# Kernel tuning notes

Hardware: AMD Instinct MI355X
Metric: run time of the kernel (lower is better)

Reference implementation:

```python
import jax, jax.numpy as jnp
import numpy as np

INF = 1e10
D_KEY = 64

def setup_inputs() -> dict:
    key = jax.random.key(0)
    k1, k2, k3 = jax.random.split(key, 3)
    B, S, D = 4, 4096, D_KEY
    return {
        "query": jax.random.normal(k1, (B, S, D), dtype=jnp.float32),
        "key": jax.random.normal(k2, (B, S, D), dtype=jnp.float32),
        "value": jax.random.normal(k3, (B, S, D), dtype=jnp.float32),
        "mask": jnp.ones((B, S), dtype=jnp.float32),
    }

def reference(query, key, value, mask):
    # dot_products: [B, Sq, Sk]
    dot = jnp.einsum('bqd,bkd->bqk', query, key)
    S = key.shape[1]
    # causal: subtract INF on strict upper triangle (triu(1))
    tri = jnp.triu(jnp.ones((S, S), dtype=dot.dtype), 1) * INF
    dot = dot - tri[None, :, :]
    # additive padding mask: subtract (1-mask)*INF broadcast over query dim
    dot = dot - (1.0 - mask)[:, None, :] * INF
    scale = jnp.sqrt(jnp.float32(D_KEY))
    probs = jax.nn.softmax(dot / scale, axis=-1)  # [B, Sq, Sk]
    # dropout ratio = 0.0 -> identity
    return jnp.einsum('bqk,bkd->bqd', probs, value)
```

## Files before the change

kernel.cpp:

```cpp
#include <hip/hip_runtime.h>
#include <hip/hip_bf16.h>


#define S_LEN  4096
#define N_B    4
#define NT64   64
#define BIGF   1.803368e9f
#define QSCALE (0.125f * 1.44269504089f)
#define FIXMAX 11.0f
#define BIGNEG 1.25e9f
#define MADD_PAD 4224

typedef __attribute__((ext_vector_type(8))) short short8;
typedef __attribute__((ext_vector_type(4))) float f32x4;
typedef __attribute__((ext_vector_type(2))) unsigned int uint2v;
typedef unsigned short ushort_t;

#define KT2_OFF   0
#define KT2_BYTES (N_B * NT64 * 4096 * 2)
#define VT2_OFF   (KT2_OFF + KT2_BYTES)
#define VT2_BYTES (N_B * NT64 * 4096 * 2)
#define NSLOT     (N_B * 368 * 4)
#define OP_OFF    (VT2_OFF + VT2_BYTES)
#define OP_BYTES  (NSLOT * 512 * 4)
#define PLS_OFF   (OP_OFF + OP_BYTES)
#define PLS_BYTES (NSLOT * 16 * 4)
#define MADD_OFF  (PLS_OFF + PLS_BYTES)
#define MADD_BYTES (N_B * MADD_PAD * 4)
#define FLAG_OFF  (MADD_OFF + MADD_BYTES)
#define WS5_NEEDED (FLAG_OFF + 64)

__device__ __forceinline__ unsigned short f2bf(float f) {
    union { float f; unsigned u; } v; v.f = f;
    unsigned r = v.u + 0x7FFF + ((v.u >> 16) & 1);
    return (unsigned short)(r >> 16);
}
__device__ __forceinline__ float bflo(unsigned u) {
    union { unsigned u; float f; } v; v.u = u << 16; return v.f;
}
__device__ __forceinline__ float bfhi(unsigned u) {
    union { unsigned u; float f; } v; v.u = u & 0xffff0000u; return v.f;
}
__device__ __forceinline__ void ld_lds16(const void* g, void* l) {
    __builtin_amdgcn_global_load_lds((const __attribute__((address_space(1))) void*)g,
                                     (__attribute__((address_space(3))) void*)l, 16, 0, 0);
}


__global__ __launch_bounds__(256)
void prep5(const float* __restrict__ K, const float* __restrict__ V,
           const float* __restrict__ M,
           ushort_t* __restrict__ Kt, ushort_t* __restrict__ Vt,
           float* __restrict__ Madd, unsigned* __restrict__ Flag)
{
    const int t = blockIdx.x, b = blockIdx.y, tid = threadIdx.x;
    ushort_t* ko = Kt + ((size_t)(b * NT64 + t)) * 4096;
    ushort_t* vo = Vt + ((size_t)(b * NT64 + t)) * 4096;
    #pragma unroll
    for (int i = 0; i < 2; ++i) {
        const int idx = tid + 256 * i;
        const int row = idx >> 3, cc = idx & 7;
        const float* src = K + ((size_t)(b * S_LEN + t * 64 + row)) * 64 + cc * 8;
        const f32x4 a = *(const f32x4*)src;
        const f32x4 d4 = *(const f32x4*)(src + 4);
        short8 w;
        w[0]=(short)f2bf(a[0]); w[1]=(short)f2bf(a[1]); w[2]=(short)f2bf(a[2]); w[3]=(short)f2bf(a[3]);
        w[4]=(short)f2bf(d4[0]); w[5]=(short)f2bf(d4[1]); w[6]=(short)f2bf(d4[2]); w[7]=(short)f2bf(d4[3]);
        *(short8*)(ko + row * 64 + ((cc ^ (row & 7)) << 3)) = w;
    }
    #pragma unroll
    for (int i = 0; i < 2; ++i) {
        const int idx = tid + 256 * i;
        const int cc = idx >> 6, d = idx & 63;
        short8 w;
        #pragma unroll
        for (int j = 0; j < 8; ++j)
            w[j] = (short)f2bf(V[((size_t)(b * S_LEN + t * 64 + cc * 8 + j)) * 64 + d]);
        *(short8*)(vo + d * 64 + ((cc ^ (d & 7)) << 3)) = w;
    }
    if (tid < 64) {
        const int k = t * 64 + tid;
        const float mv = M[b * S_LEN + k];
        Madd[b * MADD_PAD + k] = (1.0f - mv) * BIGF;
        const unsigned long long nz = __ballot(mv != 1.0f);
        if (tid == 0 && nz) atomicOr(Flag, 1u);
    }
}

#define PTRANS(PA, PB, PF) do {                                                     \
    unsigned c00_, c01_, c10_, c11_;                                                \
    __asm__("v_cvt_pk_bf16_f32 %0, %1, %2" : "=v"(c00_) : "v"(PA[0]), "v"(PA[1])); \
    __asm__("v_cvt_pk_bf16_f32 %0, %1, %2" : "=v"(c01_) : "v"(PA[2]), "v"(PA[3])); \
    __asm__("v_cvt_pk_bf16_f32 %0, %1, %2" : "=v"(c10_) : "v"(PB[0]), "v"(PB[1])); \
    __asm__("v_cvt_pk_bf16_f32 %0, %1, %2" : "=v"(c11_) : "v"(PB[2]), "v"(PB[3])); \
    uint2v s0_ = __builtin_amdgcn_permlane32_swap(c00_, c10_, false, false);        \
    uint2v s1_ = __builtin_amdgcn_permlane32_swap(c01_, c11_, false, false);        \
    const unsigned T0_ = (unsigned)__builtin_amdgcn_ds_swizzle((int)s0_.x, 0x401F); \
    const unsigned T1_ = (unsigned)__builtin_amdgcn_ds_swizzle((int)s1_.x, 0x401F); \
    const unsigned U0_ = (unsigned)__builtin_amdgcn_ds_swizzle((int)s0_.y, 0x401F); \
    const unsigned U1_ = (unsigned)__builtin_amdgcn_ds_swizzle((int)s1_.y, 0x401F); \
    union { unsigned u[4]; short8 s; } pw_;                                         \
    pw_.u[0] = evn ? s0_.x : U0_;                                                   \
    pw_.u[1] = evn ? s1_.x : U1_;                                                   \
    pw_.u[2] = evn ? T0_ : s0_.y;                                                   \
    pw_.u[3] = evn ? T1_ : s1_.y;                                                   \
    PF = pw_.s;                                                                     \
} while (0)

__global__ __launch_bounds__(256)
void attn_fa8(const float* __restrict__ Q, const ushort_t* __restrict__ Kt,
              const ushort_t* __restrict__ Vt, const float* __restrict__ Madd,
              const unsigned* __restrict__ Flag,
              unsigned* __restrict__ Opu, float* __restrict__ Pll,
              float* __restrict__ O)
{
    const int x = 373 - blockIdx.x;
    const int b = blockIdx.y;
    int v = 1;
    #pragma unroll
    for (int vv = 2; vv <= 11; ++vv) v += (x >= 3 * vv * (vv - 1)) ? 1 : 0;
    const int y  = x - 3 * v * (v - 1);
    const int T  = 6 * (v - 1) + y / v;
    const int c  = y - (y / v) * v;
    const int t0 = 6 * c;
    const int tmax = T + 1;
    const int t1 = (t0 + 6 < tmax) ? t0 + 6 : tmax;

    const unsigned anymask = *Flag;

    const int wid  = threadIdx.x >> 6;
    const int lane = threadIdx.x & 63, l15 = lane & 15, g = lane >> 4;
    const bool evn = ((lane & 16) == 0);
    const int qbase = T * 64 + wid * 16;

    __shared__ __attribute__((aligned(16))) ushort_t Kb[2][4096];
    __shared__ __attribute__((aligned(16))) ushort_t Vb[2][4096];

    const float* Qrow = Q + ((size_t)(b * S_LEN + qbase + l15)) * 64 + g * 8;
    const f32x4 qa = *(const f32x4*)(Qrow);
    const f32x4 qb_ = *(const f32x4*)(Qrow + 4);
    const f32x4 qc = *(const f32x4*)(Qrow + 32);
    const f32x4 qd = *(const f32x4*)(Qrow + 36);
    short8 qf0, qf1;
    #pragma unroll
    for (int j = 0; j < 4; ++j) {
        qf0[j]     = (short)f2bf(qa[j]  * QSCALE);
        qf0[4 + j] = (short)f2bf(qb_[j] * QSCALE);
        qf1[j]     = (short)f2bf(qc[j]  * QSCALE);
        qf1[4 + j] = (short)f2bf(qd[j]  * QSCALE);
    }
    short8 ones8;
    #pragma unroll
    for (int j = 0; j < 8; ++j) ones8[j] = (short)0x3F80;

    const char*  KtB = (const char*)Kt + (size_t)b * (NT64 * 8192);
    const char*  VtB = (const char*)Vt + (size_t)b * (NT64 * 8192);
    const float* MaB = Madd + (size_t)b * MADD_PAD + 4 * g;

    f32x4 acc[5];
    #pragma unroll
    for (int dt = 0; dt < 5; ++dt) acc[dt] = (f32x4){0.f, 0.f, 0.f, 0.f};

    auto stage = [&](int bf, int t_) {
        const char* kg = KtB + (size_t)t_ * 8192 + wid * 2048 + lane * 16;
        char* kl = (char*)&Kb[bf][0] + wid * 2048;
        ld_lds16(kg,        kl);
        ld_lds16(kg + 1024, kl + 1024);
        const char* vg = VtB + (size_t)t_ * 8192 + wid * 2048 + lane * 16;
        char* vl = (char*)&Vb[bf][0] + wid * 2048;
        ld_lds16(vg,        vl);
        ld_lds16(vg + 1024, vl + 1024);
    };

    stage(0, t0);
    int buf = 0;
    const int ch0 = ((g ^ (l15 & 7)) << 3);
    const int ch1 = (((4 | g) ^ (l15 & 7)) << 3);

    for (int t = t0; t < t1; ++t) {
        f32x4 mm0, mm1, mm2, mm3;
        if (anymask) {
            const float* mp = MaB + t * 64;
            mm0 = *(const f32x4*)(mp);
            mm1 = *(const f32x4*)(mp + 16);
            mm2 = *(const f32x4*)(mp + 32);
            mm3 = *(const f32x4*)(mp + 48);
        }
        if (t + 1 < t1) {
            stage(buf ^ 1, t + 1);
            __asm__ volatile("s_waitcnt vmcnt(4)" ::: "memory");
        } else {
            __asm__ volatile("s_waitcnt vmcnt(0)" ::: "memory");
        }
        __builtin_amdgcn_s_barrier();
        __builtin_amdgcn_sched_barrier(0);

        const ushort_t* kb = &Kb[buf][0];
        const f32x4 z_ = (f32x4){0.f, 0.f, 0.f, 0.f};
        short8 k00 = *(const short8*)(kb + ((0  + l15) << 6) + ch0);
        short8 k01 = *(const short8*)(kb + ((0  + l15) << 6) + ch1);
        short8 k10 = *(const short8*)(kb + ((16 + l15) << 6) + ch0);
        short8 k11 = *(const short8*)(kb + ((16 + l15) << 6) + ch1);
        short8 k20 = *(const short8*)(kb + ((32 + l15) << 6) + ch0);
        short8 k21 = *(const short8*)(kb + ((32 + l15) << 6) + ch1);
        short8 k30 = *(const short8*)(kb + ((48 + l15) << 6) + ch0);
        short8 k31 = *(const short8*)(kb + ((48 + l15) << 6) + ch1);
        f32x4 st0 = __builtin_amdgcn_mfma_f32_16x16x32_bf16(k00, qf0, z_, 0, 0, 0);
        f32x4 st1 = __builtin_amdgcn_mfma_f32_16x16x32_bf16(k10, qf0, z_, 0, 0, 0);
        f32x4 st2 = __builtin_amdgcn_mfma_f32_16x16x32_bf16(k20, qf0, z_, 0, 0, 0);
        f32x4 st3 = __builtin_amdgcn_mfma_f32_16x16x32_bf16(k30, qf0, z_, 0, 0, 0);
        st0 = __builtin_amdgcn_mfma_f32_16x16x32_bf16(k01, qf1, st0, 0, 0, 0);
        st1 = __builtin_amdgcn_mfma_f32_16x16x32_bf16(k11, qf1, st1, 0, 0, 0);
        st2 = __builtin_amdgcn_mfma_f32_16x16x32_bf16(k21, qf1, st2, 0, 0, 0);
        st3 = __builtin_amdgcn_mfma_f32_16x16x32_bf16(k31, qf1, st3, 0, 0, 0);

        if (anymask) {
            st0 -= mm0; st1 -= mm1; st2 -= mm2; st3 -= mm3;
        }
        if (t == T) {
            const int qg = 16 * wid + l15 - 4 * g;
            #pragma unroll
            for (int r = 0; r < 4; ++r) {
                if (r > qg)      st0[r] -= BIGF;
                if (16 + r > qg) st1[r] -= BIGF;
                if (32 + r > qg) st2[r] -= BIGF;
                if (48 + r > qg) st3[r] -= BIGF;
            }
        }

        float p0[4], p1[4], p2[4], p3[4];
        #pragma unroll
        for (int r = 0; r < 4; ++r) {
            p0[r] = exp2f(st0[r] - FIXMAX);
            p1[r] = exp2f(st1[r] - FIXMAX);
            p2[r] = exp2f(st2[r] - FIXMAX);
            p3[r] = exp2f(st3[r] - FIXMAX);
        }

        short8 pfA, pfB;
        PTRANS(p0, p1, pfA);
        PTRANS(p2, p3, pfB);

        const ushort_t* vb = &Vb[buf][0];
        short8 vA0 = *(const short8*)(vb + ((0  + l15) << 6) + ch0);
        short8 vB0 = *(const short8*)(vb + ((0  + l15) << 6) + ch1);
        short8 vA1 = *(const short8*)(vb + ((16 + l15) << 6) + ch0);
        short8 vB1 = *(const short8*)(vb + ((16 + l15) << 6) + ch1);
        short8 vA2 = *(const short8*)(vb + ((32 + l15) << 6) + ch0);
        short8 vB2 = *(const short8*)(vb + ((32 + l15) << 6) + ch1);
        short8 vA3 = *(const short8*)(vb + ((48 + l15) << 6) + ch0);
        short8 vB3 = *(const short8*)(vb + ((48 + l15) << 6) + ch1);
        __builtin_amdgcn_s_setprio(1);
        acc[0] = __builtin_amdgcn_mfma_f32_16x16x32_bf16(pfA, vA0, acc[0], 0, 0, 0);
        acc[1] = __builtin_amdgcn_mfma_f32_16x16x32_bf16(pfA, vA1, acc[1], 0, 0, 0);
        acc[2] = __builtin_amdgcn_mfma_f32_16x16x32_bf16(pfA, vA2, acc[2], 0, 0, 0);
        acc[3] = __builtin_amdgcn_mfma_f32_16x16x32_bf16(pfA, vA3, acc[3], 0, 0, 0);
        acc[4] = __builtin_amdgcn_mfma_f32_16x16x32_bf16(pfA, ones8, acc[4], 0, 0, 0);
        acc[0] = __builtin_amdgcn_mfma_f32_16x16x32_bf16(pfB, vB0, acc[0], 0, 0, 0);
        acc[1] = __builtin_amdgcn_mfma_f32_16x16x32_bf16(pfB, vB1, acc[1], 0, 0, 0);
        acc[2] = __builtin_amdgcn_mfma_f32_16x16x32_bf16(pfB, vB2, acc[2], 0, 0, 0);
        acc[3] = __builtin_amdgcn_mfma_f32_16x16x32_bf16(pfB, vB3, acc[3], 0, 0, 0);
        acc[4] = __builtin_amdgcn_mfma_f32_16x16x32_bf16(pfB, ones8, acc[4], 0, 0, 0);
        __builtin_amdgcn_s_setprio(0);

        __builtin_amdgcn_sched_barrier(0);
        __builtin_amdgcn_s_barrier();
        buf ^= 1;
    }

    if (v == 1) {
        float* Ob = O + ((size_t)(b * S_LEN + qbase)) * 64;
        #pragma unroll
        for (int r = 0; r < 4; ++r) {
            const float il = 1.0f / acc[4][r];
            #pragma unroll
            for (int dt = 0; dt < 4; ++dt)
                Ob[(4 * g + r) * 64 + 16 * dt + l15] = acc[dt][r] * il;
        }
    } else {
        const int slot = (b * 368 + (x - 6)) * 4 + wid;
        unsigned* Os = Opu + (size_t)slot * 512;
        #pragma unroll
        for (int dt = 0; dt < 4; ++dt) {
            unsigned plo, phi;
            __asm__("v_cvt_pk_bf16_f32 %0, %1, %2" : "=v"(plo) : "v"(acc[dt][0]), "v"(acc[dt][1]));
            __asm__("v_cvt_pk_bf16_f32 %0, %1, %2" : "=v"(phi) : "v"(acc[dt][2]), "v"(acc[dt][3]));
            *(uint2v*)&Os[(16 * dt + l15) * 8 + g * 2] = (uint2v){plo, phi};
        }
        if (l15 == 0) {
            #pragma unroll
            for (int r = 0; r < 4; ++r)
                Pll[slot * 16 + 4 * g + r] = acc[4][r];
        }
    }
}

__global__ __launch_bounds__(256)
void combine5(const unsigned* __restrict__ Opu, const float* __restrict__ Pll,
              float* __restrict__ O)
{
    const int bx = blockIdx.x, b = blockIdx.y;
    const int T = 6 + (bx >> 2), w = bx & 3;
    const int v = (T + 6) / 6;
    const int x0 = 3 * v * (v - 1) + (T - 6 * (v - 1)) * v;
    const int sb = (b * 368 + (x0 - 6)) * 4 + w;
    const int tid = threadIdx.x, rg = tid >> 6, d = tid & 63;

    float l[4] = {0.f, 0.f, 0.f, 0.f};
    float a[4] = {0.f, 0.f, 0.f, 0.f};
    for (int cc = 0; cc < v; ++cc) {
        const int sl = sb + 4 * cc;
        #pragma unroll
        for (int j = 0; j < 4; ++j)
            l[j] += Pll[sl * 16 + 4 * rg + j];
        const uint2v pu = *(const uint2v*)&Opu[(size_t)sl * 512 + d * 8 + rg * 2];
        a[0] += bflo(pu[0]);
        a[1] += bfhi(pu[0]);
        a[2] += bflo(pu[1]);
        a[3] += bfhi(pu[1]);
    }
    float* Ob = O + ((size_t)(b * S_LEN + T * 64 + w * 16 + 4 * rg)) * 64 + d;
    #pragma unroll
    for (int j = 0; j < 4; ++j)
        Ob[(size_t)j * 64] = a[j] / l[j];
}


__global__ __launch_bounds__(256)
void attn_fwd_fb(const float* __restrict__ Q, const float* __restrict__ K,
                 const float* __restrict__ V, const float* __restrict__ M,
                 float* __restrict__ O)
{
    const int tile  = blockIdx.x;
    const int b     = blockIdx.y;
    const int qbase = tile * 64;
    const int tid   = threadIdx.x;
    const int wave  = tid >> 6;
    const int lane  = tid & 63;
    const int l15   = lane & 15;
    const int g     = lane >> 4;

    __shared__ __attribute__((aligned(16))) unsigned short Klds[32 * 64];
    __shared__ __attribute__((aligned(16))) unsigned short Vtlds[64 * 40];
    __shared__ __attribute__((aligned(16))) unsigned short Plds[4][16 * 40];

    const float* Qb = Q + ((size_t)b * S_LEN + qbase) * 64;
    const float* Kb = K + (size_t)b * S_LEN * 64;
    const float* Vb = V + (size_t)b * S_LEN * 64;
    const float* Mb = M + (size_t)b * S_LEN;

    const int qrow = 16 * wave + l15;
    short8 qf[2];
    #pragma unroll
    for (int dc = 0; dc < 2; ++dc) {
        const float* src = Qb + (size_t)qrow * 64 + dc * 32 + g * 8;
        #pragma unroll
        for (int j = 0; j < 8; ++j) qf[dc][j] = (short)f2bf(src[j] * 0.125f);
    }

    f32x4 acc[4];
    #pragma unroll
    for (int dt = 0; dt < 4; ++dt) acc[dt] = (f32x4){0.f, 0.f, 0.f, 0.f};
    float mrow[4], lrow[4];
    #pragma unroll
    for (int r = 0; r < 4; ++r) { mrow[r] = -1e30f; lrow[r] = 0.f; }

    const int q_max_wave = qbase + 16 * wave + 15;
    const int nkv = (qbase + 64) / 32;

    for (int it = 0; it < nkv; ++it) {
        const int kv = it * 32;
        __syncthreads();
        {
            const int k = tid >> 3, c = tid & 7;
            const float* src = Kb + (size_t)(kv + k) * 64 + c * 8;
            short8 t8;
            #pragma unroll
            for (int j = 0; j < 8; ++j) t8[j] = (short)f2bf(src[j]);
            const int byte = k * 128 + ((c * 16) ^ ((k & 7) << 4));
            *(short8*)((char*)Klds + byte) = t8;
        }
        {
            const int k = tid & 31, dch = tid >> 5;
            const float* src = Vb + (size_t)(kv + k) * 64 + dch * 8;
            #pragma unroll
            for (int j = 0; j < 8; ++j)
                Vtlds[(dch * 8 + j) * 40 + k] = f2bf(src[j]);
        }
        __syncthreads();

        if (kv > q_max_wave) continue;

        f32x4 s[2];
        s[0] = (f32x4){0.f,0.f,0.f,0.f};
        s[1] = (f32x4){0.f,0.f,0.f,0.f};
        #pragma unroll
        for (int kt = 0; kt < 2; ++kt) {
            const int krow = 16 * kt + l15;
            #pragma unroll
            for (int dc = 0; dc < 2; ++dc) {
                const int byte = krow * 128 + ((dc * 64 + g * 16) ^ ((krow & 7) << 4));
                short8 kf = *(const short8*)((const char*)Klds + byte);
                s[kt] = __builtin_amdgcn_mfma_f32_16x16x32_bf16(qf[dc], kf, s[kt], 0, 0, 0);
            }
        }

        float mk0 = Mb[kv + l15];
        float mk1 = Mb[kv + 16 + l15];
        #pragma unroll
        for (int kt = 0; kt < 2; ++kt) {
            const int gk = kv + 16 * kt + l15;
            const float madd = (1.0f - (kt ? mk1 : mk0)) * BIGNEG;
            #pragma unroll
            for (int r = 0; r < 4; ++r) {
                const int gq = qbase + 16 * wave + 4 * g + r;
                float vv = s[kt][r] - madd;
                if (gk > gq) vv -= BIGNEG;
                s[kt][r] = vv;
            }
        }

        float pexp[2][4], alpha[4];
        #pragma unroll
        for (int r = 0; r < 4; ++r) {
            float tm = fmaxf(s[0][r], s[1][r]);
            #pragma unroll
            for (int off = 8; off >= 1; off >>= 1)
                tm = fmaxf(tm, __shfl_xor(tm, off, 64));
            const float mnew = fmaxf(mrow[r], tm);
            const float a  = __expf(mrow[r] - mnew);
            const float p0 = __expf(s[0][r] - mnew);
            const float p1 = __expf(s[1][r] - mnew);
            float rs = p0 + p1;
            #pragma unroll
            for (int off = 8; off >= 1; off >>= 1)
                rs += __shfl_xor(rs, off, 64);
            lrow[r] = lrow[r] * a + rs;
            mrow[r] = mnew;
            alpha[r] = a;
            pexp[0][r] = p0; pexp[1][r] = p1;
        }

        #pragma unroll
        for (int dt = 0; dt < 4; ++dt)
            #pragma unroll
            for (int r = 0; r < 4; ++r)
                acc[dt][r] *= alpha[r];

        unsigned short* P = Plds[wave];
        #pragma unroll
        for (int kt = 0; kt < 2; ++kt)
            #pragma unroll
            for (int r = 0; r < 4; ++r)
                P[(4 * g + r) * 40 + 16 * kt + l15] = f2bf(pexp[kt][r]);

        __asm__ volatile("s_waitcnt lgkmcnt(0)" ::: "memory");

        short8 pf = *(const short8*)((const char*)P + (l15 * 40 + g * 8) * 2);
        #pragma unroll
        for (int dt = 0; dt < 4; ++dt) {
            short8 vf = *(const short8*)((const char*)Vtlds + ((dt * 16 + l15) * 40 + g * 8) * 2);
            acc[dt] = __builtin_amdgcn_mfma_f32_16x16x32_bf16(pf, vf, acc[dt], 0, 0, 0);
        }
    }

    float* Ob = O + ((size_t)b * S_LEN + qbase) * 64;
    #pragma unroll
    for (int r = 0; r < 4; ++r) {
        const float inv = 1.0f / lrow[r];
        const int row = 16 * wave + 4 * g + r;
        #pragma unroll
        for (int dt = 0; dt < 4; ++dt)
            Ob[(size_t)row * 64 + dt * 16 + l15] = acc[dt][r] * inv;
    }
}

extern "C" void kernel_launch(void* const* d_in, const int* in_sizes, int n_in,
                              void* d_out, int out_size, void* d_ws, size_t ws_size,
                              hipStream_t stream) {
    const float* Q = (const float*)d_in[0];
    const float* K = (const float*)d_in[1];
    const float* V = (const float*)d_in[2];
    const float* M = (const float*)d_in[3];
    float* O = (float*)d_out;

    if (ws_size >= (size_t)WS5_NEEDED) {
        ushort_t* Kt = (ushort_t*)((char*)d_ws + KT2_OFF);
        ushort_t* Vt = (ushort_t*)((char*)d_ws + VT2_OFF);
        unsigned* Op = (unsigned*)((char*)d_ws + OP_OFF);
        float*    Pll= (float*)((char*)d_ws + PLS_OFF);
        float*    Ma = (float*)((char*)d_ws + MADD_OFF);
        unsigned* Fl = (unsigned*)((char*)d_ws + FLAG_OFF);
        hipMemsetAsync(Fl, 0, 4, stream);
        prep5<<<dim3(NT64, N_B), 256, 0, stream>>>(K, V, M, Kt, Vt, Ma, Fl);
        attn_fa8<<<dim3(374, N_B), 256, 0, stream>>>(Q, Kt, Vt, Ma, Fl, Op, Pll, O);
        combine5<<<dim3(232, N_B), 256, 0, stream>>>(Op, Pll, O);
    } else {
        dim3 grid(S_LEN / 64, N_B);
        attn_fwd_fb<<<grid, 256, 0, stream>>>(Q, K, V, M, O);
    }
}
```

Measured before the change: 45.59 us.

## Use 128-row query tiles with 8 waves and a triple-buffered K/V pipeline

Moves the main attention kernel to 512-thread blocks that each cover 128 query rows, so every staged K/V tile is reused by eight waves instead of four, which halves the number of work items. Global-to-LDS staging becomes a three-slot ring with a prefetch distance of two and one barrier per tile. The padding-mask additive is now staged into LDS and always applied, which removes the host memset and the any-mask flag path. Waves whose diagonal tile comes before the block's last tile skip compute on the final tile. The costs are larger blocks with more LDS per block, idle waves on the diagonal, and a changed split and combine layout.

```diff
diff --git a/kernel.cpp b/kernel.cpp
--- a/kernel.cpp
+++ b/kernel.cpp
@@ -20,15 +20,14 @@
 #define KT2_BYTES (N_B * NT64 * 4096 * 2)
 #define VT2_OFF   (KT2_OFF + KT2_BYTES)
 #define VT2_BYTES (N_B * NT64 * 4096 * 2)
-#define NSLOT     (N_B * 368 * 4)
+#define NSLOT     (N_B * 184 * 8)
 #define OP_OFF    (VT2_OFF + VT2_BYTES)
 #define OP_BYTES  (NSLOT * 512 * 4)
 #define PLS_OFF   (OP_OFF + OP_BYTES)
 #define PLS_BYTES (NSLOT * 16 * 4)
 #define MADD_OFF  (PLS_OFF + PLS_BYTES)
 #define MADD_BYTES (N_B * MADD_PAD * 4)
-#define FLAG_OFF  (MADD_OFF + MADD_BYTES)
-#define WS5_NEEDED (FLAG_OFF + 64)
+#define WS8_NEEDED (MADD_OFF + MADD_BYTES)
 
 __device__ __forceinline__ unsigned short f2bf(float f) {
     union { float f; unsigned u; } v; v.f = f;
@@ -45,13 +44,17 @@
     __builtin_amdgcn_global_load_lds((const __attribute__((address_space(1))) void*)g,
                                      (__attribute__((address_space(3))) void*)l, 16, 0, 0);
 }
+__device__ __forceinline__ void ld_lds4(const void* g, void* l) {
+    __builtin_amdgcn_global_load_lds((const __attribute__((address_space(1))) void*)g,
+                                     (__attribute__((address_space(3))) void*)l, 4, 0, 0);
+}
 
 
 __global__ __launch_bounds__(256)
-void prep5(const float* __restrict__ K, const float* __restrict__ V,
+void prep6(const float* __restrict__ K, const float* __restrict__ V,
            const float* __restrict__ M,
            ushort_t* __restrict__ Kt, ushort_t* __restrict__ Vt,
-           float* __restrict__ Madd, unsigned* __restrict__ Flag)
+           float* __restrict__ Madd)
 {
     const int t = blockIdx.x, b = blockIdx.y, tid = threadIdx.x;
     ushort_t* ko = Kt + ((size_t)(b * NT64 + t)) * 4096;
@@ -80,10 +83,7 @@
     }
     if (tid < 64) {
         const int k = t * 64 + tid;
-        const float mv = M[b * S_LEN + k];
-        Madd[b * MADD_PAD + k] = (1.0f - mv) * BIGF;
-        const unsigned long long nz = __ballot(mv != 1.0f);
-        if (tid == 0 && nz) atomicOr(Flag, 1u);
+        Madd[b * MADD_PAD + k] = (1.0f - M[b * S_LEN + k]) * BIGF;
     }
 }
 
@@ -107,40 +107,46 @@
     PF = pw_.s;                                                                     \
 } while (0)
 
-__global__ __launch_bounds__(256)
-void attn_fa8(const float* __restrict__ Q, const ushort_t* __restrict__ Kt,
-              const ushort_t* __restrict__ Vt, const float* __restrict__ Madd,
-              const unsigned* __restrict__ Flag,
-              unsigned* __restrict__ Opu, float* __restrict__ Pll,
-              float* __restrict__ O)
+#define CMASK(SV, BB, QG) do {                     \
+    _Pragma("unroll")                              \
+    for (int r_ = 0; r_ < 4; ++r_)                 \
+        if ((BB) + r_ > (QG)) SV[r_] -= BIGF;      \
+} while (0)
+
+__global__ __launch_bounds__(512, 6)
+void attn_fa11(const float* __restrict__ Q, const ushort_t* __restrict__ Kt,
+               const ushort_t* __restrict__ Vt, const float* __restrict__ Madd,
+               unsigned* __restrict__ Opu, float* __restrict__ Pll,
+               float* __restrict__ O)
 {
-    const int x = 373 - blockIdx.x;
+    const int x = 186 - blockIdx.x;
     const int b = blockIdx.y;
     int v = 1;
     #pragma unroll
-    for (int vv = 2; vv <= 11; ++vv) v += (x >= 3 * vv * (vv - 1)) ? 1 : 0;
-    const int y  = x - 3 * v * (v - 1);
-    const int T  = 6 * (v - 1) + y / v;
+    for (int vv = 2; vv <= 11; ++vv) v += (x >= (3 * vv * (vv - 1)) / 2) ? 1 : 0;
+    const int y  = x - (3 * v * (v - 1)) / 2;
+    const int T  = 3 * (v - 1) + y / v;
     const int c  = y - (y / v) * v;
+    const int nt = 2 * T + 2;
     const int t0 = 6 * c;
-    const int tmax = T + 1;
-    const int t1 = (t0 + 6 < tmax) ? t0 + 6 : tmax;
-
-    const unsigned anymask = *Flag;
+    const int t1 = (t0 + 6 < nt) ? t0 + 6 : nt;
 
     const int wid  = threadIdx.x >> 6;
     const int lane = threadIdx.x & 63, l15 = lane & 15, g = lane >> 4;
     const bool evn = ((lane & 16) == 0);
-    const int qbase = T * 64 + wid * 16;
-
-    __shared__ __attribute__((aligned(16))) ushort_t Kb[2][4096];
-    __shared__ __attribute__((aligned(16))) ushort_t Vb[2][4096];
+    const int qbase = T * 128 + wid * 16;
+    const int dtile = 2 * T + (wid >> 2);
+    const int qg = 16 * (wid & 3) + l15 - 4 * g;
+
+    __shared__ __attribute__((aligned(16))) ushort_t Kb[3][4096];
+    __shared__ __attribute__((aligned(16))) ushort_t Vb[3][4096];
+    __shared__ __attribute__((aligned(16))) float    Ml[3][64];
 
     const float* Qrow = Q + ((size_t)(b * S_LEN + qbase + l15)) * 64 + g * 8;
-    const f32x4 qa = *(const f32x4*)(Qrow);
+    const f32x4 qa  = *(const f32x4*)(Qrow);
     const f32x4 qb_ = *(const f32x4*)(Qrow + 4);
-    const f32x4 qc = *(const f32x4*)(Qrow + 32);
-    const f32x4 qd = *(const f32x4*)(Qrow + 36);
+    const f32x4 qc  = *(const f32x4*)(Qrow + 32);
+    const f32x4 qd  = *(const f32x4*)(Qrow + 36);
     short8 qf0, qf1;
     #pragma unroll
     for (int j = 0; j < 4; ++j) {
@@ -153,119 +159,110 @@
     #pragma unroll
     for (int j = 0; j < 8; ++j) ones8[j] = (short)0x3F80;
 
-    const char*  KtB = (const char*)Kt + (size_t)b * (NT64 * 8192);
-    const char*  VtB = (const char*)Vt + (size_t)b * (NT64 * 8192);
-    const float* MaB = Madd + (size_t)b * MADD_PAD + 4 * g;
+    const char*  KtB  = (const char*)Kt + (size_t)b * (NT64 * 8192);
+    const char*  VtB  = (const char*)Vt + (size_t)b * (NT64 * 8192);
+    const float* MaBs = Madd + (size_t)b * MADD_PAD;
 
     f32x4 acc[5];
     #pragma unroll
     for (int dt = 0; dt < 5; ++dt) acc[dt] = (f32x4){0.f, 0.f, 0.f, 0.f};
 
-    auto stage = [&](int bf, int t_) {
-        const char* kg = KtB + (size_t)t_ * 8192 + wid * 2048 + lane * 16;
-        char* kl = (char*)&Kb[bf][0] + wid * 2048;
-        ld_lds16(kg,        kl);
-        ld_lds16(kg + 1024, kl + 1024);
-        const char* vg = VtB + (size_t)t_ * 8192 + wid * 2048 + lane * 16;
-        char* vl = (char*)&Vb[bf][0] + wid * 2048;
-        ld_lds16(vg,        vl);
-        ld_lds16(vg + 1024, vl + 1024);
+    auto stage = [&](int sl, int t_) {
+        ld_lds16(KtB + (size_t)t_ * 8192 + wid * 1024 + lane * 16,
+                 (char*)&Kb[sl][0] + wid * 1024);
+        ld_lds16(VtB + (size_t)t_ * 8192 + wid * 1024 + lane * 16,
+                 (char*)&Vb[sl][0] + wid * 1024);
+        if (wid == 0)
+            ld_lds4(MaBs + (size_t)t_ * 64 + lane, &Ml[sl][0]);
     };
 
     stage(0, t0);
-    int buf = 0;
+    if (t0 + 1 < t1) stage(1, t0 + 1);
+
     const int ch0 = ((g ^ (l15 & 7)) << 3);
     const int ch1 = (((4 | g) ^ (l15 & 7)) << 3);
 
+    int sc = 0;
     for (int t = t0; t < t1; ++t) {
-        f32x4 mm0, mm1, mm2, mm3;
-        if (anymask) {
-            const float* mp = MaB + t * 64;
-            mm0 = *(const f32x4*)(mp);
-            mm1 = *(const f32x4*)(mp + 16);
-            mm2 = *(const f32x4*)(mp + 32);
-            mm3 = *(const f32x4*)(mp + 48);
-        }
         if (t + 1 < t1) {
-            stage(buf ^ 1, t + 1);
-            __asm__ volatile("s_waitcnt vmcnt(4)" ::: "memory");
+            if (wid == 0) __asm__ volatile("s_waitcnt vmcnt(3)" ::: "memory");
+            else          __asm__ volatile("s_waitcnt vmcnt(2)" ::: "memory");
         } else {
             __asm__ volatile("s_waitcnt vmcnt(0)" ::: "memory");
         }
         __builtin_amdgcn_s_barrier();
         __builtin_amdgcn_sched_barrier(0);
 
-        const ushort_t* kb = &Kb[buf][0];
-        const f32x4 z_ = (f32x4){0.f, 0.f, 0.f, 0.f};
-        short8 k00 = *(const short8*)(kb + ((0  + l15) << 6) + ch0);
-        short8 k01 = *(const short8*)(kb + ((0  + l15) << 6) + ch1);
-        short8 k10 = *(const short8*)(kb + ((16 + l15) << 6) + ch0);
-        short8 k11 = *(const short8*)(kb + ((16 + l15) << 6) + ch1);
-        short8 k20 = *(const short8*)(kb + ((32 + l15) << 6) + ch0);
-        short8 k21 = *(const short8*)(kb + ((32 + l15) << 6) + ch1);
-        short8 k30 = *(const short8*)(kb + ((48 + l15) << 6) + ch0);
-        short8 k31 = *(const short8*)(kb + ((48 + l15) << 6) + ch1);
-        f32x4 st0 = __builtin_amdgcn_mfma_f32_16x16x32_bf16(k00, qf0, z_, 0, 0, 0);
-        f32x4 st1 = __builtin_amdgcn_mfma_f32_16x16x32_bf16(k10, qf0, z_, 0, 0, 0);
-        f32x4 st2 = __builtin_amdgcn_mfma_f32_16x16x32_bf16(k20, qf0, z_, 0, 0, 0);
-        f32x4 st3 = __builtin_amdgcn_mfma_f32_16x16x32_bf16(k30, qf0, z_, 0, 0, 0);
-        st0 = __builtin_amdgcn_mfma_f32_16x16x32_bf16(k01, qf1, st0, 0, 0, 0);
-        st1 = __builtin_amdgcn_mfma_f32_16x16x32_bf16(k11, qf1, st1, 0, 0, 0);
-        st2 = __builtin_amdgcn_mfma_f32_16x16x32_bf16(k21, qf1, st2, 0, 0, 0);
-        st3 = __builtin_amdgcn_mfma_f32_16x16x32_bf16(k31, qf1, st3, 0, 0, 0);
-
-        if (anymask) {
-            st0 -= mm0; st1 -= mm1; st2 -= mm2; st3 -= mm3;
-        }
-        if (t == T) {
-            const int qg = 16 * wid + l15 - 4 * g;
+        const int sn = (sc + 2 > 2) ? sc - 1 : sc + 2;
+        if (t + 2 < t1) stage(sn, t + 2);
+
+        if (t <= dtile) {
+            const ushort_t* kb  = &Kb[sc][0];
+            const ushort_t* vb  = &Vb[sc][0];
+            const float*    mlw = &Ml[sc][0];
+            const f32x4 z_ = (f32x4){0.f, 0.f, 0.f, 0.f};
+
+            short8 k00 = *(const short8*)(kb + ((0  + l15) << 6) + ch0);
+            short8 k01 = *(const short8*)(kb + ((0  + l15) << 6) + ch1);
+            short8 k10 = *(const short8*)(kb + ((16 + l15) << 6) + ch0);
+            short8 k11 = *(const short8*)(kb + ((16 + l15) << 6) + ch1);
+            short8 k20 = *(const short8*)(kb + ((32 + l15) << 6) + ch0);
+            short8 k21 = *(const short8*)(kb + ((32 + l15) << 6) + ch1);
+            short8 k30 = *(const short8*)(kb + ((48 + l15) << 6) + ch0);
+            short8 k31 = *(const short8*)(kb + ((48 + l15) << 6) + ch1);
+            f32x4 st0 = __builtin_amdgcn_mfma_f32_16x16x32_bf16(k00, qf0, z_, 0, 0, 0);
+            f32x4 st1 = __builtin_amdgcn_mfma_f32_16x16x32_bf16(k10, qf0, z_, 0, 0, 0);
+            f32x4 st2 = __builtin_amdgcn_mfma_f32_16x16x32_bf16(k20, qf0, z_, 0, 0, 0);
+            f32x4 st3 = __builtin_amdgcn_mfma_f32_16x16x32_bf16(k30, qf0, z_, 0, 0, 0);
+            st0 = __builtin_amdgcn_mfma_f32_16x16x32_bf16(k01, qf1, st0, 0, 0, 0);
+            st1 = __builtin_amdgcn_mfma_f32_16x16x32_bf16(k11, qf1, st1, 0, 0, 0);
+            st2 = __builtin_amdgcn_mfma_f32_16x16x32_bf16(k21, qf1, st2, 0, 0, 0);
+            st3 = __builtin_amdgcn_mfma_f32_16x16x32_bf16(k31, qf1, st3, 0, 0, 0);
+
+            st0 -= *(const f32x4*)(mlw + 4 * g);
+            st1 -= *(const f32x4*)(mlw + 16 + 4 * g);
+            st2 -= *(const f32x4*)(mlw + 32 + 4 * g);
+            st3 -= *(const f32x4*)(mlw + 48 + 4 * g);
+            if (t == dtile) {
+                CMASK(st0, 0, qg);  CMASK(st1, 16, qg);
+                CMASK(st2, 32, qg); CMASK(st3, 48, qg);
+            }
+
+            float p0[4], p1[4], p2[4], p3[4];
             #pragma unroll
             for (int r = 0; r < 4; ++r) {
-                if (r > qg)      st0[r] -= BIGF;
-                if (16 + r > qg) st1[r] -= BIGF;
-                if (32 + r > qg) st2[r] -= BIGF;
-                if (48 + r > qg) st3[r] -= BIGF;
+                p0[r] = exp2f(st0[r] - FIXMAX);
+                p1[r] = exp2f(st1[r] - FIXMAX);
+                p2[r] = exp2f(st2[r] - FIXMAX);
+                p3[r] = exp2f(st3[r] - FIXMAX);
             }
-        }
-
-        float p0[4], p1[4], p2[4], p3[4];
-        #pragma unroll
-        for (int r = 0; r < 4; ++r) {
-            p0[r] = exp2f(st0[r] - FIXMAX);
-            p1[r] = exp2f(st1[r] - FIXMAX);
-            p2[r] = exp2f(st2[r] - FIXMAX);
-            p3[r] = exp2f(st3[r] - FIXMAX);
-        }
-
-        short8 pfA, pfB;
-        PTRANS(p0, p1, pfA);
-        PTRANS(p2, p3, pfB);
-
-        const ushort_t* vb = &Vb[buf][0];
-        short8 vA0 = *(const short8*)(vb + ((0  + l15) << 6) + ch0);
-        short8 vB0 = *(const short8*)(vb + ((0  + l15) << 6) + ch1);
-        short8 vA1 = *(const short8*)(vb + ((16 + l15) << 6) + ch0);
-        short8 vB1 = *(const short8*)(vb + ((16 + l15) << 6) + ch1);
-        short8 vA2 = *(const short8*)(vb + ((32 + l15) << 6) + ch0);
-        short8 vB2 = *(const short8*)(vb + ((32 + l15) << 6) + ch1);
-        short8 vA3 = *(const short8*)(vb + ((48 + l15) << 6) + ch0);
-        short8 vB3 = *(const short8*)(vb + ((48 + l15) << 6) + ch1);
-        __builtin_amdgcn_s_setprio(1);
-        acc[0] = __builtin_amdgcn_mfma_f32_16x16x32_bf16(pfA, vA0, acc[0], 0, 0, 0);
-        acc[1] = __builtin_amdgcn_mfma_f32_16x16x32_bf16(pfA, vA1, acc[1], 0, 0, 0);
-        acc[2] = __builtin_amdgcn_mfma_f32_16x16x32_bf16(pfA, vA2, acc[2], 0, 0, 0);
-        acc[3] = __builtin_amdgcn_mfma_f32_16x16x32_bf16(pfA, vA3, acc[3], 0, 0, 0);
-        acc[4] = __builtin_amdgcn_mfma_f32_16x16x32_bf16(pfA, ones8, acc[4], 0, 0, 0);
-        acc[0] = __builtin_amdgcn_mfma_f32_16x16x32_bf16(pfB, vB0, acc[0], 0, 0, 0);
-        acc[1] = __builtin_amdgcn_mfma_f32_16x16x32_bf16(pfB, vB1, acc[1], 0, 0, 0);
-        acc[2] = __builtin_amdgcn_mfma_f32_16x16x32_bf16(pfB, vB2, acc[2], 0, 0, 0);
-        acc[3] = __builtin_amdgcn_mfma_f32_16x16x32_bf16(pfB, vB3, acc[3], 0, 0, 0);
-        acc[4] = __builtin_amdgcn_mfma_f32_16x16x32_bf16(pfB, ones8, acc[4], 0, 0, 0);
-        __builtin_amdgcn_s_setprio(0);
-
-        __builtin_amdgcn_sched_barrier(0);
-        __builtin_amdgcn_s_barrier();
-        buf ^= 1;
+
+            short8 pfA, pfB;
+            PTRANS(p0, p1, pfA);
+            PTRANS(p2, p3, pfB);
+
+            short8 vA0 = *(const short8*)(vb + ((0  + l15) << 6) + ch0);
+            short8 vB0 = *(const short8*)(vb + ((0  + l15) << 6) + ch1);
+            short8 vA1 = *(const short8*)(vb + ((16 + l15) << 6) + ch0);
+            short8 vB1 = *(const short8*)(vb + ((16 + l15) << 6) + ch1);
+            short8 vA2 = *(const short8*)(vb + ((32 + l15) << 6) + ch0);
+            short8 vB2 = *(const short8*)(vb + ((32 + l15) << 6) + ch1);
+            short8 vA3 = *(const short8*)(vb + ((48 + l15) << 6) + ch0);
+            short8 vB3 = *(const short8*)(vb + ((48 + l15) << 6) + ch1);
+            __builtin_amdgcn_s_setprio(1);
+            acc[0] = __builtin_amdgcn_mfma_f32_16x16x32_bf16(pfA, vA0, acc[0], 0, 0, 0);
+            acc[1] = __builtin_amdgcn_mfma_f32_16x16x32_bf16(pfA, vA1, acc[1], 0, 0, 0);
+            acc[2] = __builtin_amdgcn_mfma_f32_16x16x32_bf16(pfA, vA2, acc[2], 0, 0, 0);
+            acc[3] = __builtin_amdgcn_mfma_f32_16x16x32_bf16(pfA, vA3, acc[3], 0, 0, 0);
+            acc[4] = __builtin_amdgcn_mfma_f32_16x16x32_bf16(pfA, ones8, acc[4], 0, 0, 0);
+            acc[0] = __builtin_amdgcn_mfma_f32_16x16x32_bf16(pfB, vB0, acc[0], 0, 0, 0);
+            acc[1] = __builtin_amdgcn_mfma_f32_16x16x32_bf16(pfB, vB1, acc[1], 0, 0, 0);
+            acc[2] = __builtin_amdgcn_mfma_f32_16x16x32_bf16(pfB, vB2, acc[2], 0, 0, 0);
+            acc[3] = __builtin_amdgcn_mfma_f32_16x16x32_bf16(pfB, vB3, acc[3], 0, 0, 0);
+            acc[4] = __builtin_amdgcn_mfma_f32_16x16x32_bf16(pfB, ones8, acc[4], 0, 0, 0);
+            __builtin_amdgcn_s_setprio(0);
+        }
+        sc = (sc == 2) ? 0 : sc + 1;
     }
 
     if (v == 1) {
@@ -278,7 +275,7 @@
                 Ob[(4 * g + r) * 64 + 16 * dt + l15] = acc[dt][r] * il;
         }
     } else {
-        const int slot = (b * 368 + (x - 6)) * 4 + wid;
+        const int slot = (b * 184 + (x - 3)) * 8 + wid;
         unsigned* Os = Opu + (size_t)slot * 512;
         #pragma unroll
         for (int dt = 0; dt < 4; ++dt) {
@@ -296,30 +293,30 @@
 }
 
 __global__ __launch_bounds__(256)
-void combine5(const unsigned* __restrict__ Opu, const float* __restrict__ Pll,
+void combine7(const unsigned* __restrict__ Opu, const float* __restrict__ Pll,
               float* __restrict__ O)
 {
     const int bx = blockIdx.x, b = blockIdx.y;
-    const int T = 6 + (bx >> 2), w = bx & 3;
-    const int v = (T + 6) / 6;
-    const int x0 = 3 * v * (v - 1) + (T - 6 * (v - 1)) * v;
-    const int sb = (b * 368 + (x0 - 6)) * 4 + w;
+    const int T = 3 + (bx >> 3), wv = bx & 7;
+    const int v = (T + 3) / 3;
+    const int x0 = (3 * v * (v - 1)) / 2 + (T - 3 * (v - 1)) * v;
+    const int sb = (b * 184 + (x0 - 3)) * 8 + wv;
     const int tid = threadIdx.x, rg = tid >> 6, d = tid & 63;
 
     float l[4] = {0.f, 0.f, 0.f, 0.f};
     float a[4] = {0.f, 0.f, 0.f, 0.f};
     for (int cc = 0; cc < v; ++cc) {
-        const int sl = sb + 4 * cc;
-        #pragma unroll
-        for (int j = 0; j < 4; ++j)
-            l[j] += Pll[sl * 16 + 4 * rg + j];
+        const int sl = sb + 8 * cc;
         const uint2v pu = *(const uint2v*)&Opu[(size_t)sl * 512 + d * 8 + rg * 2];
         a[0] += bflo(pu[0]);
         a[1] += bfhi(pu[0]);
         a[2] += bflo(pu[1]);
         a[3] += bfhi(pu[1]);
-    }
-    float* Ob = O + ((size_t)(b * S_LEN + T * 64 + w * 16 + 4 * rg)) * 64 + d;
+        #pragma unroll
+        for (int j = 0; j < 4; ++j)
+            l[j] += Pll[sl * 16 + 4 * rg + j];
+    }
+    float* Ob = O + ((size_t)(b * S_LEN + T * 128 + wv * 16 + 4 * rg)) * 64 + d;
     #pragma unroll
     for (int j = 0; j < 4; ++j)
         Ob[(size_t)j * 64] = a[j] / l[j];
@@ -484,17 +481,15 @@
     const float* M = (const float*)d_in[3];
     float* O = (float*)d_out;
 
-    if (ws_size >= (size_t)WS5_NEEDED) {
+    if (ws_size >= (size_t)WS8_NEEDED) {
         ushort_t* Kt = (ushort_t*)((char*)d_ws + KT2_OFF);
         ushort_t* Vt = (ushort_t*)((char*)d_ws + VT2_OFF);
         unsigned* Op = (unsigned*)((char*)d_ws + OP_OFF);
         float*    Pll= (float*)((char*)d_ws + PLS_OFF);
         float*    Ma = (float*)((char*)d_ws + MADD_OFF);
-        unsigned* Fl = (unsigned*)((char*)d_ws + FLAG_OFF);
-        hipMemsetAsync(Fl, 0, 4, stream);
-        prep5<<<dim3(NT64, N_B), 256, 0, stream>>>(K, V, M, Kt, Vt, Ma, Fl);
-        attn_fa8<<<dim3(374, N_B), 256, 0, stream>>>(Q, Kt, Vt, Ma, Fl, Op, Pll, O);
-        combine5<<<dim3(232, N_B), 256, 0, stream>>>(Op, Pll, O);
+        prep6<<<dim3(NT64, N_B), 256, 0, stream>>>(K, V, M, Kt, Vt, Ma);
+        attn_fa11<<<dim3(187, N_B), 512, 0, stream>>>(Q, Kt, Vt, Ma, Op, Pll, O);
+        combine7<<<dim3(232, N_B), 256, 0, stream>>>(Op, Pll, O);
     } else {
         dim3 grid(S_LEN / 64, N_B);
         attn_fwd_fb<<<grid, 256, 0, stream>>>(Q, K, V, M, O);
```

Result: faster. 43.37 us (-4.9%).
